# Kernel optimization log

Hardware: AMD Instinct MI355X
Metric: run time of the kernel (lower is better)

## Reference

```python
import jax, jax.numpy as jnp
import numpy as np

RADII = (3, 5, 7)      # window_levels
S, B, D = 1024, 8, 512  # seq_len, batch, feature_dim
EPS = 1e-12             # F.normalize eps


def setup_inputs() -> dict:
    key = jax.random.key(0)
    k0, k1, k2 = jax.random.split(key, 3)
    x = jax.random.normal(k0, (S, B, D), jnp.float32)          # seq-first like the torch path
    W = jax.random.normal(k1, (3, D, D), jnp.float32) / np.sqrt(D)  # 3 level linear weights
    b = jax.random.normal(k2, (3, D), jnp.float32) * 0.01           # 3 level linear biases
    alphas = jnp.ones((3,), jnp.float32)   # nn.Parameter(torch.ones)
    betas = jnp.zeros((3,), jnp.float32)   # nn.Parameter(torch.zeros)
    return {"x": x, "W": W, "b": b, "alphas": alphas, "betas": betas}


def reference(x, W, b, alphas, betas):
    # x: [S, B, D] (seq-first). torch code transposes to [B, S, D], works, transposes back.
    # Dropout is identity (eval mode). output = x + sum over levels of per-timestep
    # windowed, similarity-weighted sums of linearly transformed neighbors; all
    # windows read the ORIGINAL x, so levels are independent additive terms.
    xb = jnp.transpose(x, (1, 0, 2))  # [B, S, D]
    Bn, Sn, Dn = xb.shape
    dt = xb.dtype
    # L2-normalized features (F.normalize with eps=1e-12)
    xnorm = xb / jnp.maximum(jnp.linalg.norm(xb, axis=-1, keepdims=True), EPS)
    # prefix sums for O(1) window means (edge-truncated windows)
    csum = jnp.concatenate([jnp.zeros((Bn, 1, Dn), dt), jnp.cumsum(xb, axis=1)], axis=1)
    t_idx = jnp.arange(Sn)
    out = xb
    for m, r in enumerate(RADII):
        starts = jnp.clip(t_idx - r, 0, Sn)        # [S]
        ends = jnp.clip(t_idx + r + 1, 0, Sn)      # [S]
        cnt = (ends - starts).astype(dt)           # window sizes (truncated at edges)
        center = (csum[:, ends, :] - csum[:, starts, :]) / cnt[None, :, None]  # [B,S,D]
        cnorm = center / jnp.maximum(jnp.linalg.norm(center, axis=-1, keepdims=True), EPS)
        # sliding-window gather indices, masked at sequence edges
        offs = jnp.arange(-r, r + 1)
        pos = t_idx[:, None] + offs[None, :]       # [S, w]
        valid = ((pos >= 0) & (pos < Sn)).astype(dt)
        idx = jnp.clip(pos, 0, Sn - 1)
        nw = xnorm[:, idx, :]                      # [B, S, w, D]
        sim = jnp.einsum('bswd,bsd->bsw', nw, cnorm)  # cosine similarity to window mean
        wts = jax.nn.sigmoid(alphas[m] * sim + betas[m]) * valid[None, :, :]
        tfm = xb @ W[m].T + b[m]                   # level-m linear transform, computed once
        tw = tfm[:, idx, :]                        # [B, S, w, D]
        out = out + jnp.einsum('bsw,bswd->bsd', wts, tw)
    return jnp.transpose(out, (1, 0, 2))  # back to [S, B, D]
```

## Files before the change

kernel.cpp:

```cpp
#include <hip/hip_runtime.h>

typedef __attribute__((ext_vector_type(8))) short short8;
typedef __attribute__((ext_vector_type(4))) float f32x4;

#define S_LEN 1024
#define B_N 8
#define D_DIM 512
#define SLAB 4194304

static __device__ __forceinline__ unsigned short f2bf(float f){
  unsigned int u = __float_as_uint(f);
  u = u + 0x7fffu + ((u>>16)&1u);
  return (unsigned short)(u>>16);
}
static __device__ __forceinline__ float bf2f(unsigned short h){
  return __uint_as_float(((unsigned int)h)<<16);
}

#define GLL16(g,l) __builtin_amdgcn_global_load_lds( \
    (__attribute__((address_space(1))) void*)(g), \
    (__attribute__((address_space(3))) void*)(l), 16, 0, 0)

__global__ __launch_bounds__(256) void k_conv_x(const float* __restrict__ x,
    unsigned short* __restrict__ xbf, float* __restrict__ invn)
{
  int row = blockIdx.x, tid = threadIdx.x;
  size_t off = (size_t)row*D_DIM + tid*2;
  float2 v = *(const float2*)(x + off);
  ushort2 h; h.x = f2bf(v.x); h.y = f2bf(v.y);
  *(ushort2*)(xbf + off) = h;
  float ss = v.x*v.x + v.y*v.y;
  for (int o=32;o;o>>=1) ss += __shfl_down(ss,o,64);
  __shared__ float red[4];
  if ((tid&63)==0) red[tid>>6] = ss;
  __syncthreads();
  if (tid==0) invn[row] = 1.0f/fmaxf(sqrtf(red[0]+red[1]+red[2]+red[3]), 1e-12f);
}

__global__ __launch_bounds__(256) void k_conv_w(const float* __restrict__ Wsrc,
    unsigned short* __restrict__ wbf)
{
  int i = (blockIdx.x*256 + threadIdx.x)*4;
  float4 v = *(const float4*)(Wsrc + i);
  ushort4 h;
  h.x = f2bf(v.x); h.y = f2bf(v.y); h.z = f2bf(v.z); h.w = f2bf(v.w);
  *(ushort4*)(wbf + i) = h;
}

__global__ __launch_bounds__(256) void k_gemm(const unsigned short* __restrict__ A,
    const unsigned short* __restrict__ Bw, const float* __restrict__ bias,
    unsigned short* __restrict__ C)
{
  __shared__ __align__(16) unsigned short smem[16384];
  unsigned short* As = smem;
  unsigned short* Bs = smem + 4096;
  int bx = blockIdx.x % 12, by = blockIdx.x / 12;
  int tid = threadIdx.x, lane = tid & 63, w = tid >> 6;
  int wm = w >> 1, wn = w & 1;
  int c0 = w*128 + lane, c1 = c0 + 64;
  const unsigned short* gA0 = A + (size_t)(by*128 + (c0>>2))*512 + (c0&3)*8;
  const unsigned short* gA1 = A + (size_t)(by*128 + (c1>>2))*512 + (c1&3)*8;
  const unsigned short* gB0 = Bw + (size_t)(bx*128 + (c0>>2))*512 + (c0&3)*8;
  const unsigned short* gB1 = Bw + (size_t)(bx*128 + (c1>>2))*512 + (c1&3)*8;
  unsigned short* lA0 = As + (w*2+0)*512;
  unsigned short* lA1 = As + (w*2+1)*512;
  unsigned short* lB0 = Bs + (w*2+0)*512;
  unsigned short* lB1 = Bs + (w*2+1)*512;
  f32x4 acc[4][4];
  #pragma unroll
  for (int i=0;i<4;++i)
    #pragma unroll
    for (int j=0;j<4;++j)
      acc[i][j] = (f32x4){0.f,0.f,0.f,0.f};
  int lane15 = lane & 15, klo = (lane>>4)*8;
  for (int kt=0; kt<16; ++kt){
    GLL16(gA0, lA0); GLL16(gA1, lA1); GLL16(gB0, lB0); GLL16(gB1, lB1);
    gA0 += 32; gA1 += 32; gB0 += 32; gB1 += 32;
    __syncthreads();
    short8 af[4], bfr[4];
    #pragma unroll
    for (int i=0;i<4;++i)
      af[i] = *(const short8*)(As + (wm*64 + i*16 + lane15)*32 + klo);
    #pragma unroll
    for (int j=0;j<4;++j)
      bfr[j] = *(const short8*)(Bs + (wn*64 + j*16 + lane15)*32 + klo);
    #pragma unroll
    for (int i=0;i<4;++i)
      #pragma unroll
      for (int j=0;j<4;++j)
        acc[i][j] = __builtin_amdgcn_mfma_f32_16x16x32_bf16(af[i], bfr[j], acc[i][j], 0,0,0);
    __syncthreads();
  }
  int rbase = (lane>>4)*4;
  #pragma unroll
  for (int j=0;j<4;++j){
    int nl = wn*64 + j*16 + lane15;
    float bv = bias[bx*128 + nl];
    #pragma unroll
    for (int i=0;i<4;++i){
      int rl0 = wm*64 + i*16 + rbase;
      #pragma unroll
      for (int rg=0;rg<4;++rg)
        smem[(rl0+rg)*128 + nl] = f2bf(acc[i][j][rg] + bv);
    }
  }
  __syncthreads();
  int m_r = bx >> 2, colb = (bx&3)*128;
  #pragma unroll
  for (int p=0;p<8;++p){
    int R = p*16 + (tid>>4);
    int ch = (tid&15)*8;
    uint4 v = *(const uint4*)(smem + R*128 + ch);
    *(uint4*)(C + (size_t)m_r*SLAB + (size_t)(by*128 + R)*512 + colb + ch) = v;
  }
}

__global__ __launch_bounds__(192) void k_gram(const unsigned short* __restrict__ xbf,
    float* __restrict__ Gband)
{
  int blk = blockIdx.x;
  int b = blk & 7, i0 = (blk >> 3) * 16;
  int tid = threadIdx.x, lane = tid & 63, w = tid >> 6;
  int j0 = i0 + (w - 1) * 16;
  if (j0 < 0 || j0 >= S_LEN) return;
  int l15 = lane & 15, klo = (lane >> 4) * 8;
  const unsigned short* Ar = xbf + ((size_t)(i0 + l15) * B_N + b) * D_DIM + klo;
  const unsigned short* Br = xbf + ((size_t)(j0 + l15) * B_N + b) * D_DIM + klo;
  f32x4 acc = (f32x4){0.f,0.f,0.f,0.f};
  #pragma unroll
  for (int kt = 0; kt < 16; ++kt){
    short8 af = *(const short8*)(Ar + kt*32);
    short8 bf = *(const short8*)(Br + kt*32);
    acc = __builtin_amdgcn_mfma_f32_16x16x32_bf16(af, bf, acc, 0,0,0);
  }
  int rb = (lane >> 4) * 4;
  #pragma unroll
  for (int rg = 0; rg < 4; ++rg){
    int i = i0 + rb + rg;
    int j = j0 + l15;
    int dl = j - i;
    if (dl >= -14 && dl <= 14)
      Gband[((size_t)b * S_LEN + i) * 32 + dl + 14] = acc[rg];
  }
}

__global__ __launch_bounds__(256) void k_wts(const float* __restrict__ Gband,
    const float* __restrict__ invn, const float* __restrict__ alphas,
    const float* __restrict__ betas, float* __restrict__ wts)
{
  int blk = blockIdx.x;
  int b = blk & 7, tg = blk >> 3;
  int tid = threadIdx.x, lane = tid & 63, wid = tid >> 6;
  int t = tg * 4 + wid;
  __shared__ float pshare[4][33];
  __shared__ float invc[4][3];
  int p = lane;
  float pp = 0.f; int m = 0, pos = 0, valid = 0;
  if (p < 33){
    int r, wsl;
    if (p < 7){ m = 0; r = 3; wsl = p; }
    else if (p < 18){ m = 1; r = 5; wsl = p - 7; }
    else { m = 2; r = 7; wsl = p - 18; }
    pos = t + wsl - r;
    valid = (pos >= 0 && pos < S_LEN);
    if (valid){
      int ulo = max(t - r, 0), uhi = min(t + r, S_LEN - 1);
      size_t base = ((size_t)b * S_LEN + pos) * 32;
      for (int u = ulo; u <= uhi; ++u)
        pp += Gband[base + (u - pos + 14)];
    }
    pshare[wid][p] = valid ? pp : 0.f;
  }
  __syncthreads();
  if (lane < 3){
    int s0 = lane == 0 ? 0 : (lane == 1 ? 7 : 18);
    int c  = lane == 0 ? 7 : (lane == 1 ? 11 : 15);
    float s = 0.f;
    for (int k = 0; k < c; ++k) s += pshare[wid][s0 + k];
    invc[wid][lane] = 1.0f / fmaxf(sqrtf(s), 1e-12f);
  }
  __syncthreads();
  if (p < 33){
    float wt = 0.f;
    if (valid){
      float sim = pp * invn[pos * B_N + b] * invc[wid][m];
      float z = alphas[m] * sim + betas[m];
      wt = 1.0f / (1.0f + expf(-z));
    }
    wts[((size_t)t * B_N + b) * 33 + p] = wt;
  }
}

__global__ __launch_bounds__(256) void k_gath(const float* __restrict__ x,
    const unsigned short* __restrict__ tfm, const float* __restrict__ wts,
    float* __restrict__ out)
{
  int blk = blockIdx.x;
  int b = blk & 7, tg = blk >> 3;
  int tid = threadIdx.x, h = tid >> 7, j = tid & 127;
  int t = tg * 2 + h;
  __shared__ float wsh[2][33];
  if (j < 33) wsh[h][j] = wts[((size_t)t * B_N + b) * 33 + j];
  __syncthreads();
  int d0 = j * 4;
  size_t xoff = ((size_t)t * B_N + b) * D_DIM + d0;
  float4 a = *(const float4*)(x + xoff);
  float ax = a.x, ay = a.y, az = a.z, aw = a.w;
  #pragma unroll
  for (int p = 0; p < 33; ++p){
    int m, r, wsl;
    if (p < 7){ m = 0; r = 3; wsl = p; }
    else if (p < 18){ m = 1; r = 5; wsl = p - 7; }
    else { m = 2; r = 7; wsl = p - 18; }
    int pos = t + wsl - r;
    if (pos < 0 || pos >= S_LEN) continue;
    float wt = wsh[h][p];
    const unsigned short* tp = tfm + (size_t)m * SLAB + ((size_t)pos * B_N + b) * D_DIM + d0;
    uint2 uv = *(const uint2*)tp;
    ax += wt * bf2f((unsigned short)(uv.x & 0xffffu));
    ay += wt * bf2f((unsigned short)(uv.x >> 16));
    az += wt * bf2f((unsigned short)(uv.y & 0xffffu));
    aw += wt * bf2f((unsigned short)(uv.y >> 16));
  }
  *(float4*)(out + xoff) = make_float4(ax, ay, az, aw);
}

extern "C" void kernel_launch(void* const* d_in, const int* in_sizes, int n_in,
                              void* d_out, int out_size, void* d_ws, size_t ws_size,
                              hipStream_t stream) {
  const float* x      = (const float*)d_in[0];
  const float* W      = (const float*)d_in[1];
  const float* bias   = (const float*)d_in[2];
  const float* alphas = (const float*)d_in[3];
  const float* betas  = (const float*)d_in[4];
  float* out = (float*)d_out;
  char* ws = (char*)d_ws;
  unsigned short* xbf  = (unsigned short*)ws;
  unsigned short* wbf  = (unsigned short*)(ws + 8388608);
  float*          invn = (float*)(ws + 8388608 + 1572864);
  unsigned short* tfm  = (unsigned short*)(ws + 8388608 + 1572864 + 32768);
  float*          Gband= (float*)(ws + 8388608 + 1572864 + 32768 + 25165824);
  float*          wts  = (float*)(ws + 8388608 + 1572864 + 32768 + 25165824 + 1048576);

  k_conv_x<<<8192, 256, 0, stream>>>(x, xbf, invn);
  k_conv_w<<<768, 256, 0, stream>>>(W, wbf);
  k_gram<<<512, 192, 0, stream>>>(xbf, Gband);
  k_gemm<<<768, 256, 0, stream>>>(xbf, wbf, bias, tfm);
  k_wts<<<2048, 256, 0, stream>>>(Gband, invn, alphas, betas, wts);
  k_gath<<<4096, 256, 0, stream>>>(x, tfm, wts, out);
}
```

Measured before the change: 73.48 us.

## Fuse six launches into three: merged convert, gemm+gram, weights into gather

Merges the x and W bf16 conversions into one kernel and drops the separate norm reduction, taking each row's inverse norm from the Gram diagonal instead. The Gram band computation is appended as extra blocks of the GEMM launch so both run concurrently. The sigmoid weight computation is folded into the gather kernel, which removes the wts buffer round trip and three launches. The norm now comes from bf16-rounded dot products rather than fp32, which slightly changes numerics.

```diff
diff --git a/kernel.cpp b/kernel.cpp
--- a/kernel.cpp
+++ b/kernel.cpp
@@ -7,6 +7,8 @@
 #define B_N 8
 #define D_DIM 512
 #define SLAB 4194304
+#define NX   4194304
+#define NW   786432
 
 static __device__ __forceinline__ unsigned short f2bf(float f){
   unsigned int u = __float_as_uint(f);
@@ -21,41 +23,58 @@
     (__attribute__((address_space(1))) void*)(g), \
     (__attribute__((address_space(3))) void*)(l), 16, 0, 0)
 
-__global__ __launch_bounds__(256) void k_conv_x(const float* __restrict__ x,
-    unsigned short* __restrict__ xbf, float* __restrict__ invn)
-{
-  int row = blockIdx.x, tid = threadIdx.x;
-  size_t off = (size_t)row*D_DIM + tid*2;
-  float2 v = *(const float2*)(x + off);
-  ushort2 h; h.x = f2bf(v.x); h.y = f2bf(v.y);
-  *(ushort2*)(xbf + off) = h;
-  float ss = v.x*v.x + v.y*v.y;
-  for (int o=32;o;o>>=1) ss += __shfl_down(ss,o,64);
-  __shared__ float red[4];
-  if ((tid&63)==0) red[tid>>6] = ss;
-  __syncthreads();
-  if (tid==0) invn[row] = 1.0f/fmaxf(sqrtf(red[0]+red[1]+red[2]+red[3]), 1e-12f);
-}
-
-__global__ __launch_bounds__(256) void k_conv_w(const float* __restrict__ Wsrc,
+__global__ __launch_bounds__(256) void k_conv(const float* __restrict__ x,
+    const float* __restrict__ W, unsigned short* __restrict__ xbf,
     unsigned short* __restrict__ wbf)
 {
-  int i = (blockIdx.x*256 + threadIdx.x)*4;
-  float4 v = *(const float4*)(Wsrc + i);
+  size_t i = ((size_t)blockIdx.x*256 + threadIdx.x)*4;
+  const float* src; unsigned short* dst;
+  if (i < NX){ src = x + i; dst = xbf + i; }
+  else       { src = W + (i - NX); dst = wbf + (i - NX); }
+  float4 v = *(const float4*)src;
   ushort4 h;
   h.x = f2bf(v.x); h.y = f2bf(v.y); h.z = f2bf(v.z); h.w = f2bf(v.w);
-  *(ushort4*)(wbf + i) = h;
-}
-
-__global__ __launch_bounds__(256) void k_gemm(const unsigned short* __restrict__ A,
+  *(ushort4*)dst = h;
+}
+
+__global__ __launch_bounds__(256) void k_heavy(const unsigned short* __restrict__ A,
     const unsigned short* __restrict__ Bw, const float* __restrict__ bias,
-    unsigned short* __restrict__ C)
+    unsigned short* __restrict__ C, float* __restrict__ Gband)
 {
   __shared__ __align__(16) unsigned short smem[16384];
+  int blk = blockIdx.x;
+  int tid = threadIdx.x, lane = tid & 63, w = tid >> 6;
+
+  if (blk >= 768){
+    if (w >= 3) return;
+    int g = blk - 768;
+    int b = g & 7, i0 = (g >> 3) * 16;
+    int j0 = i0 + (w - 1) * 16;
+    if (j0 < 0 || j0 >= S_LEN) return;
+    int l15 = lane & 15, klo = (lane >> 4) * 8;
+    const unsigned short* Ar = A + ((size_t)(i0 + l15) * B_N + b) * D_DIM + klo;
+    const unsigned short* Br = A + ((size_t)(j0 + l15) * B_N + b) * D_DIM + klo;
+    f32x4 acc = (f32x4){0.f,0.f,0.f,0.f};
+    #pragma unroll
+    for (int kt = 0; kt < 16; ++kt){
+      short8 af = *(const short8*)(Ar + kt*32);
+      short8 bf = *(const short8*)(Br + kt*32);
+      acc = __builtin_amdgcn_mfma_f32_16x16x32_bf16(af, bf, acc, 0,0,0);
+    }
+    int rb = (lane >> 4) * 4;
+    #pragma unroll
+    for (int rg = 0; rg < 4; ++rg){
+      int i = i0 + rb + rg;
+      int dl = j0 + l15 - i;
+      if (dl >= -14 && dl <= 14)
+        Gband[((size_t)b * S_LEN + i) * 32 + dl + 14] = acc[rg];
+    }
+    return;
+  }
+
   unsigned short* As = smem;
   unsigned short* Bs = smem + 4096;
-  int bx = blockIdx.x % 12, by = blockIdx.x / 12;
-  int tid = threadIdx.x, lane = tid & 63, w = tid >> 6;
+  int bx = blk % 12, by = blk / 12;
   int wm = w >> 1, wn = w & 1;
   int c0 = w*128 + lane, c1 = c0 + 64;
   const unsigned short* gA0 = A + (size_t)(by*128 + (c0>>2))*512 + (c0&3)*8;
@@ -115,92 +134,53 @@
   }
 }
 
-__global__ __launch_bounds__(192) void k_gram(const unsigned short* __restrict__ xbf,
-    float* __restrict__ Gband)
-{
-  int blk = blockIdx.x;
-  int b = blk & 7, i0 = (blk >> 3) * 16;
-  int tid = threadIdx.x, lane = tid & 63, w = tid >> 6;
-  int j0 = i0 + (w - 1) * 16;
-  if (j0 < 0 || j0 >= S_LEN) return;
-  int l15 = lane & 15, klo = (lane >> 4) * 8;
-  const unsigned short* Ar = xbf + ((size_t)(i0 + l15) * B_N + b) * D_DIM + klo;
-  const unsigned short* Br = xbf + ((size_t)(j0 + l15) * B_N + b) * D_DIM + klo;
-  f32x4 acc = (f32x4){0.f,0.f,0.f,0.f};
-  #pragma unroll
-  for (int kt = 0; kt < 16; ++kt){
-    short8 af = *(const short8*)(Ar + kt*32);
-    short8 bf = *(const short8*)(Br + kt*32);
-    acc = __builtin_amdgcn_mfma_f32_16x16x32_bf16(af, bf, acc, 0,0,0);
-  }
-  int rb = (lane >> 4) * 4;
-  #pragma unroll
-  for (int rg = 0; rg < 4; ++rg){
-    int i = i0 + rb + rg;
-    int j = j0 + l15;
-    int dl = j - i;
-    if (dl >= -14 && dl <= 14)
-      Gband[((size_t)b * S_LEN + i) * 32 + dl + 14] = acc[rg];
-  }
-}
-
-__global__ __launch_bounds__(256) void k_wts(const float* __restrict__ Gband,
-    const float* __restrict__ invn, const float* __restrict__ alphas,
-    const float* __restrict__ betas, float* __restrict__ wts)
-{
-  int blk = blockIdx.x;
-  int b = blk & 7, tg = blk >> 3;
-  int tid = threadIdx.x, lane = tid & 63, wid = tid >> 6;
-  int t = tg * 4 + wid;
-  __shared__ float pshare[4][33];
-  __shared__ float invc[4][3];
-  int p = lane;
-  float pp = 0.f; int m = 0, pos = 0, valid = 0;
-  if (p < 33){
-    int r, wsl;
-    if (p < 7){ m = 0; r = 3; wsl = p; }
-    else if (p < 18){ m = 1; r = 5; wsl = p - 7; }
-    else { m = 2; r = 7; wsl = p - 18; }
-    pos = t + wsl - r;
-    valid = (pos >= 0 && pos < S_LEN);
-    if (valid){
-      int ulo = max(t - r, 0), uhi = min(t + r, S_LEN - 1);
-      size_t base = ((size_t)b * S_LEN + pos) * 32;
-      for (int u = ulo; u <= uhi; ++u)
-        pp += Gband[base + (u - pos + 14)];
-    }
-    pshare[wid][p] = valid ? pp : 0.f;
-  }
-  __syncthreads();
-  if (lane < 3){
-    int s0 = lane == 0 ? 0 : (lane == 1 ? 7 : 18);
-    int c  = lane == 0 ? 7 : (lane == 1 ? 11 : 15);
-    float s = 0.f;
-    for (int k = 0; k < c; ++k) s += pshare[wid][s0 + k];
-    invc[wid][lane] = 1.0f / fmaxf(sqrtf(s), 1e-12f);
-  }
-  __syncthreads();
-  if (p < 33){
-    float wt = 0.f;
-    if (valid){
-      float sim = pp * invn[pos * B_N + b] * invc[wid][m];
-      float z = alphas[m] * sim + betas[m];
-      wt = 1.0f / (1.0f + expf(-z));
-    }
-    wts[((size_t)t * B_N + b) * 33 + p] = wt;
-  }
-}
-
 __global__ __launch_bounds__(256) void k_gath(const float* __restrict__ x,
-    const unsigned short* __restrict__ tfm, const float* __restrict__ wts,
+    const unsigned short* __restrict__ tfm, const float* __restrict__ Gband,
+    const float* __restrict__ alphas, const float* __restrict__ betas,
     float* __restrict__ out)
 {
   int blk = blockIdx.x;
   int b = blk & 7, tg = blk >> 3;
   int tid = threadIdx.x, h = tid >> 7, j = tid & 127;
   int t = tg * 2 + h;
+  __shared__ float pshare[2][33];
+  __shared__ float invc[2][3];
   __shared__ float wsh[2][33];
-  if (j < 33) wsh[h][j] = wts[((size_t)t * B_N + b) * 33 + j];
+  int m = 0, pos = 0, valid = 0;
+  float pp = 0.f, invnp = 0.f;
+  if (j < 33){
+    int r, wsl;
+    if (j < 7){ m = 0; r = 3; wsl = j; }
+    else if (j < 18){ m = 1; r = 5; wsl = j - 7; }
+    else { m = 2; r = 7; wsl = j - 18; }
+    pos = t + wsl - r;
+    valid = (pos >= 0 && pos < S_LEN);
+    if (valid){
+      const float* grow = Gband + ((size_t)b * S_LEN + pos) * 32;
+      int ulo = max(t - r, 0), uhi = min(t + r, S_LEN - 1);
+      for (int u = ulo; u <= uhi; ++u) pp += grow[u - pos + 14];
+      invnp = rsqrtf(fmaxf(grow[14], 1e-24f));
+    }
+    pshare[h][j] = valid ? pp : 0.f;
+  }
+  __syncthreads();
+  if (j < 3){
+    int s0 = j == 0 ? 0 : (j == 1 ? 7 : 18);
+    int c  = j == 0 ? 7 : (j == 1 ? 11 : 15);
+    float s = 0.f;
+    for (int k = 0; k < c; ++k) s += pshare[h][s0 + k];
+    invc[h][j] = rsqrtf(fmaxf(s, 1e-24f));
+  }
+  __syncthreads();
+  if (j < 33){
+    float wt = 0.f;
+    if (valid){
+      float sim = pp * invnp * invc[h][m];
+      float z = alphas[m] * sim + betas[m];
+      wt = 1.0f / (1.0f + expf(-z));
+    }
+    wsh[h][j] = wt;
+  }
   __syncthreads();
   int d0 = j * 4;
   size_t xoff = ((size_t)t * B_N + b) * D_DIM + d0;
@@ -208,14 +188,14 @@
   float ax = a.x, ay = a.y, az = a.z, aw = a.w;
   #pragma unroll
   for (int p = 0; p < 33; ++p){
-    int m, r, wsl;
-    if (p < 7){ m = 0; r = 3; wsl = p; }
-    else if (p < 18){ m = 1; r = 5; wsl = p - 7; }
-    else { m = 2; r = 7; wsl = p - 18; }
-    int pos = t + wsl - r;
-    if (pos < 0 || pos >= S_LEN) continue;
+    int pm, pr, wsl;
+    if (p < 7){ pm = 0; pr = 3; wsl = p; }
+    else if (p < 18){ pm = 1; pr = 5; wsl = p - 7; }
+    else { pm = 2; pr = 7; wsl = p - 18; }
+    int ppos = t + wsl - pr;
+    if (ppos < 0 || ppos >= S_LEN) continue;
     float wt = wsh[h][p];
-    const unsigned short* tp = tfm + (size_t)m * SLAB + ((size_t)pos * B_N + b) * D_DIM + d0;
+    const unsigned short* tp = tfm + (size_t)pm * SLAB + ((size_t)ppos * B_N + b) * D_DIM + d0;
     uint2 uv = *(const uint2*)tp;
     ax += wt * bf2f((unsigned short)(uv.x & 0xffffu));
     ay += wt * bf2f((unsigned short)(uv.x >> 16));
@@ -237,15 +217,10 @@
   char* ws = (char*)d_ws;
   unsigned short* xbf  = (unsigned short*)ws;
   unsigned short* wbf  = (unsigned short*)(ws + 8388608);
-  float*          invn = (float*)(ws + 8388608 + 1572864);
-  unsigned short* tfm  = (unsigned short*)(ws + 8388608 + 1572864 + 32768);
-  float*          Gband= (float*)(ws + 8388608 + 1572864 + 32768 + 25165824);
-  float*          wts  = (float*)(ws + 8388608 + 1572864 + 32768 + 25165824 + 1048576);
-
-  k_conv_x<<<8192, 256, 0, stream>>>(x, xbf, invn);
-  k_conv_w<<<768, 256, 0, stream>>>(W, wbf);
-  k_gram<<<512, 192, 0, stream>>>(xbf, Gband);
-  k_gemm<<<768, 256, 0, stream>>>(xbf, wbf, bias, tfm);
-  k_wts<<<2048, 256, 0, stream>>>(Gband, invn, alphas, betas, wts);
-  k_gath<<<4096, 256, 0, stream>>>(x, tfm, wts, out);
-}
+  unsigned short* tfm  = (unsigned short*)(ws + 8388608 + 1572864);
+  float*          Gband= (float*)(ws + 8388608 + 1572864 + 25165824);
+
+  k_conv <<<4864, 256, 0, stream>>>(x, W, xbf, wbf);
+  k_heavy<<<1280, 256, 0, stream>>>(xbf, wbf, bias, tfm, Gband);
+  k_gath <<<4096, 256, 0, stream>>>(x, tfm, Gband, alphas, betas, out);
+}
```

New measurement: 67.81 us. 1.08x faster.
